# Optimization experiments

Measured on AMD Instinct MI355X. Metric: run time of the kernel, lower is better.

Reference implementation:

```python
import jax, jax.numpy as jnp
import numpy as np

ALPHABET = 26
VGENES = 60
JGENES = 20
E = 1024      # embedding_dim (= 2*VJ + LATENT)
H = 2048      # hidden_dim
LATENT = 768  # latent_space_dim
VJ = 128      # embedding_dim_VJ
L = 4096      # sequence length
X_IDX = 23    # all_letters.index('X')
B_IDX = 1     # all_letters.index('B')


def setup_inputs() -> dict:
    key = jax.random.key(0)
    ks = jax.random.split(key, 16)
    s = lambda fan_in: 1.0 / np.sqrt(fan_in)
    u = lambda k, shape, sc: jax.random.uniform(k, shape, jnp.float32, -sc, sc)
    return {
        "x": jax.random.randint(ks[0], (L,), 0, ALPHABET, dtype=jnp.int32),
        "Vg": jax.random.randint(ks[1], (1,), 0, VGENES, dtype=jnp.int32),
        "Jg": jax.random.randint(ks[2], (1,), 0, JGENES, dtype=jnp.int32),
        "tick": 0,
        "emb": jax.random.normal(ks[3], (ALPHABET, E), jnp.float32),
        "embV": jax.random.normal(ks[4], (VGENES, VJ), jnp.float32),
        "embJ": jax.random.normal(ks[5], (JGENES, VJ), jnp.float32),
        "W_ih_enc": u(ks[6], (4 * H, E), s(H)),
        "W_hh_enc": u(ks[7], (4 * H, H), s(H)),
        "b_ih_enc": u(ks[8], (4 * H,), s(H)),
        "b_hh_enc": u(ks[9], (4 * H,), s(H)),
        "W_ls": u(ks[10], (LATENT, H), s(H)),
        "b_ls": u(ks[11], (LATENT,), s(H)),
        "W_ih_dec": u(ks[12], (4 * E, E), s(E)),
        "W_hh_dec": u(ks[13], (4 * E, E), s(E)),
        "b_ih_dec": u(ks[14], (4 * E,), s(E)),
        "b_hh_dec": u(ks[15], (4 * E,), s(E)),
    }


def _lstm_cell(x_t, h, c, W_ih, W_hh, b):
    # torch gate order: i, f, g, o
    g = x_t @ W_ih.T + h @ W_hh.T + b
    i, f, gg, o = jnp.split(g, 4, axis=-1)
    c = jax.nn.sigmoid(f) * c + jax.nn.sigmoid(i) * jnp.tanh(gg)
    h = jax.nn.sigmoid(o) * jnp.tanh(c)
    return h, c


def reference(x, Vg, Jg, tick, emb, embV, embJ,
              W_ih_enc, W_hh_enc, b_ih_enc, b_hh_enc,
              W_ls, b_ls,
              W_ih_dec, W_hh_dec, b_ih_dec, b_hh_dec):
    # ---- encode ----
    embedded = emb[x]                       # [L, E]
    b_enc = b_ih_enc + b_hh_enc

    def enc_step(carry, x_t):
        h, c = carry
        h, c = _lstm_cell(x_t, h, c, W_ih_enc, W_hh_enc, b_enc)
        return (h, c), None

    h0 = jnp.zeros((H,), embedded.dtype)
    (h_n, _), _ = jax.lax.scan(enc_step, (h0, h0), embedded)
    latent = jnp.tanh(h_n @ W_ls.T + b_ls)  # [LATENT]

    # ---- concat latent with V/J gene embeddings -> [E] ----
    latent_cat = jnp.concatenate([embV[Vg[0]], latent, embJ[Jg[0]]])

    # ---- decode: feed own output back as next input ----
    b_dec = b_ih_dec + b_hh_dec
    prev0 = emb[X_IDX]                      # start letter embedding [E]

    def dec_step(carry, _):
        prev, h, c = carry
        h, c = _lstm_cell(prev, h, c, W_ih_dec, W_hh_dec, b_dec)
        return (h, h, c), h

    (_, _, _), outs = jax.lax.scan(dec_step, (prev0, latent_cat, latent_cat),
                                   None, length=L - 2)  # [L-2, E]

    seq = jnp.concatenate([prev0[None], outs, emb[B_IDX][None]], axis=0)  # [L, E]
    recon = seq[::-1][:, None, :]           # [L, 1, E] (original reverses the list)

    return latent_cat[None, None, :], recon, embedded
```

## Files before the change

### kernel.cpp

```cpp
#include <hip/hip_runtime.h>
#include <hip/hip_bf16.h>
#include <stdint.h>

#define NWG 256
typedef unsigned long long u64;

typedef __attribute__((ext_vector_type(8))) short bf16x8;
typedef __attribute__((ext_vector_type(4))) float f32x4;

__device__ __forceinline__ short f2bf(float f) {
    unsigned u = __float_as_uint(f);
    unsigned r = (u + 0x7fffu + ((u >> 16) & 1u)) >> 16;
    return (short)r;
}

__device__ __forceinline__ void gload16(const void* g, void* l) {
    __builtin_amdgcn_global_load_lds(
        (const __attribute__((address_space(1))) void*)g,
        (__attribute__((address_space(3))) void*)l, 16, 0, 0);
}

__device__ __forceinline__ u64 ald(const u64* p) {
    return __hip_atomic_load(p, __ATOMIC_RELAXED, __HIP_MEMORY_SCOPE_AGENT);
}
__device__ __forceinline__ void ast(u64* p, u64 v) {
    __hip_atomic_store(p, v, __ATOMIC_RELAXED, __HIP_MEMORY_SCOPE_AGENT);
}
__device__ __forceinline__ u64 pack(unsigned tag, float f) {
    return ((u64)tag << 32) | (u64)(unsigned)__float_as_uint(f);
}

__global__ void prep_all(const int* __restrict__ x, const int* __restrict__ Vg, const int* __restrict__ Jg,
                         const float* __restrict__ emb, const float* __restrict__ embV, const float* __restrict__ embJ,
                         const float* __restrict__ Wih_e,
                         const float* __restrict__ Wih_d, const float* __restrict__ Whh_d,
                         float* __restrict__ out,
                         short* __restrict__ Abf, short* __restrict__ Wbf,
                         float* __restrict__ wsum,
                         u64* __restrict__ bufE, u64* __restrict__ bufD)
{
    const size_t i0 = (size_t)blockIdx.x * blockDim.x + threadIdx.x;
    const size_t str = (size_t)gridDim.x * blockDim.x;
    for (size_t i = i0; i < (size_t)4096 * 1024; i += str) {
        int t = (int)(i >> 10), j = (int)(i & 1023);
        float v = emb[(size_t)x[t] * 1024 + j];
        out[4195328 + i] = v;
        Abf[i] = f2bf(v);
    }
    for (size_t i = i0; i < (size_t)8192 * 1024; i += str) Wbf[i] = f2bf(Wih_e[i]);
    for (size_t i = i0; i < (size_t)4096 * 1024; i += str) wsum[i] = Wih_d[i] + Whh_d[i];
    for (size_t i = i0; i < 1024; i += str) {
        out[1024 + i] = emb[1 * 1024 + i];
        out[1024 + (size_t)4095 * 1024 + i] = emb[23 * 1024 + i];
    }
    for (size_t i = i0; i < 6144; i += str) bufE[i] = 0ull;
    for (size_t i = i0; i < 3072; i += str) {
        u64 v = 0ull;
        if (i < 1024) {
            if (i < 128)      v = pack(0u, embV[(size_t)Vg[0] * 128 + i]);
            else if (i < 896) v = 0xFFFFFFFF00000000ull;
            else              v = pack(0u, embJ[(size_t)Jg[0] * 128 + (i - 896)]);
        }
        bufD[i] = v;
    }
    for (size_t i = i0; i < 128; i += str) {
        out[i]       = embV[(size_t)Vg[0] * 128 + i];
        out[896 + i] = embJ[(size_t)Jg[0] * 128 + i];
    }
}

__global__ void prep_pg(const float* __restrict__ Wih_d, const float* __restrict__ emb,
                        const float* __restrict__ bih_d, const float* __restrict__ bhh_d,
                        float* __restrict__ pg)
{
    const int lane = threadIdx.x & 63, wv = threadIdx.x >> 6;
    const float* prev0 = emb + 23 * 1024;
    for (int rr = 0; rr < 16; rr++) {
        int row = blockIdx.x * 64 + wv * 16 + rr;
        float s = 0.f;
        #pragma unroll
        for (int q = 0; q < 16; q++) {
            int k = lane + q * 64;
            s += Wih_d[(size_t)row * 1024 + k] * prev0[k];
        }
        for (int o = 32; o; o >>= 1) s += __shfl_xor(s, o, 64);
        if (lane == 0) pg[row] = s + bih_d[row] + bhh_d[row];
    }
}

__launch_bounds__(256, 2)
__global__ void gemm_xgates(const short* __restrict__ A,
                            const short* __restrict__ B,
                            const float* __restrict__ bih, const float* __restrict__ bhh,
                            float* __restrict__ C)
{
    __shared__ short lA[128 * 32];
    __shared__ short lB[128 * 32];
    const int bid = blockIdx.x;
    const int mb = bid >> 6;
    const int nb = bid & 63;
    const int tid = threadIdx.x, lane = tid & 63, wv = tid >> 6;
    const int wr = wv >> 1, wc = wv & 1;
    const int Mbase = mb * 128, Nbase = nb * 128;
    f32x4 acc[4][4] = {};

    for (int kt = 0; kt < 32; kt++) {
        __syncthreads();
        const int k0b = kt * 64;
        #pragma unroll
        for (int c = 0; c < 2; c++) {
            int f = tid * 16 + c * 4096;
            int row = f >> 6, kb = f & 63;
            const char* ga = (const char*)A + (size_t)(Mbase + row) * 2048 + k0b + kb;
            const char* gb = (const char*)B + (size_t)(Nbase + row) * 2048 + k0b + kb;
            gload16(ga, (char*)lA + wv * 1024 + c * 4096);
            gload16(gb, (char*)lB + wv * 1024 + c * 4096);
        }
        asm volatile("s_waitcnt vmcnt(0)" ::: "memory");
        __syncthreads();
        bf16x8 af[4], bf[4];
        #pragma unroll
        for (int i = 0; i < 4; i++) {
            af[i] = *(const bf16x8*)&lA[(wr * 64 + i * 16 + (lane & 15)) * 32 + (lane >> 4) * 8];
            bf[i] = *(const bf16x8*)&lB[(wc * 64 + i * 16 + (lane & 15)) * 32 + (lane >> 4) * 8];
        }
        #pragma unroll
        for (int i = 0; i < 4; i++)
            #pragma unroll
            for (int j = 0; j < 4; j++)
                acc[i][j] = __builtin_amdgcn_mfma_f32_16x16x32_bf16(af[i], bf[j], acc[i][j], 0, 0, 0);
    }
    #pragma unroll
    for (int i = 0; i < 4; i++) {
        #pragma unroll
        for (int j = 0; j < 4; j++) {
            int col = Nbase + wc * 64 + j * 16 + (lane & 15);
            float bv = bih[col] + bhh[col];
            #pragma unroll
            for (int r = 0; r < 4; r++) {
                int row = Mbase + wr * 64 + i * 16 + (lane >> 4) * 4 + r;
                C[(size_t)row * 8192 + col] = acc[i][j][r] + bv;
            }
        }
    }
}

__launch_bounds__(1024, 4)
__global__ void rnn_seq(const float* __restrict__ Whh_e,
                        const float* __restrict__ Wls,
                        const float* __restrict__ bls,
                        const float* __restrict__ Whh_d,
                        const float* __restrict__ Gx,
                        const float* __restrict__ wsum,
                        const float* __restrict__ bih_d, const float* __restrict__ bhh_d,
                        const float* __restrict__ pg,
                        u64* __restrict__ bufE,
                        u64* __restrict__ bufD,
                        float* __restrict__ out)
{
    const int w = blockIdx.x;
    const int tid = threadIdx.x;
    const int lane = tid & 63, wv = tid >> 6;
    __shared__ float hl[2][2048];
    __shared__ float red[2][32];
    __shared__ float cst[8];

    float we[64];
    #pragma unroll
    for (int rr = 0; rr < 2; rr++) {
        int r = wv * 2 + rr;
        const float* src = Whh_e + (size_t)((r >> 3) * 2048 + 8 * w + (r & 7)) * 2048 + lane;
        #pragma unroll
        for (int j = 0; j < 32; j++) we[rr * 32 + j] = src[64 * j];
    }
    if (tid < 8) cst[tid] = 0.f;
    const int grow = (tid >> 3) * 2048 + 8 * w + (tid & 7);
    float gx = 0.f;
    if (tid < 32) gx = Gx[grow];
    __syncthreads();

    #pragma unroll 1
    for (int t = 0; t < 4096; t++) {
        const unsigned tg = (unsigned)t;
        const u64* p = bufE + (size_t)(t % 3) * 2048 + wv * 128 + 2 * lane;
        u64 a0 = ald(p), a1 = ald(p + 1);
        for (;;) {
            bool ok = ((unsigned)(a0 >> 32) == tg) & ((unsigned)(a1 >> 32) == tg);
            if (__builtin_expect(__all(ok), 1)) break;
            a0 = ald(p); a1 = ald(p + 1);
        }
        float2 hv = { __uint_as_float((unsigned)a0), __uint_as_float((unsigned)a1) };
        *(float2*)&hl[t & 1][wv * 128 + 2 * lane] = hv;
        __syncthreads();

        float gx_next = 0.f;
        if (tid < 32 && t < 4095) gx_next = Gx[(size_t)(t + 1) * 8192 + grow];

        float s0 = 0.f, s1 = 0.f;
        const float* hp = hl[t & 1];
        #pragma unroll
        for (int j = 0; j < 32; j++) {
            float h = hp[lane + 64 * j];
            s0 += we[j] * h;
            s1 += we[32 + j] * h;
        }
        #pragma unroll
        for (int o = 32; o; o >>= 1) {
            s0 += __shfl_xor(s0, o, 64);
            s1 += __shfl_xor(s1, o, 64);
        }
        if (lane == 0) { red[t & 1][wv * 2] = s0; red[t & 1][wv * 2 + 1] = s1; }
        __syncthreads();

        if (tid < 32) {
            float g = red[t & 1][tid] + gx;
            float gi = __shfl(g, (tid & 7), 64);
            float gf = __shfl(g, (tid & 7) + 8, 64);
            float gg = __shfl(g, (tid & 7) + 16, 64);
            float go = __shfl(g, (tid & 7) + 24, 64);
            if (tid < 8) {
                float c  = cst[tid];
                float ig = 1.f / (1.f + expf(-gi));
                float fg = 1.f / (1.f + expf(-gf));
                float og = 1.f / (1.f + expf(-go));
                float cn = fg * c + ig * tanhf(gg);
                float hn = og * tanhf(cn);
                cst[tid] = cn;
                ast(&bufE[(size_t)((t + 1) % 3) * 2048 + 8 * w + tid], pack(tg + 1, hn));
            }
        }
        gx = gx_next;
    }

    {
        const unsigned tg = 4096u;
        const u64* p = bufE + (size_t)2048 + wv * 128 + 2 * lane;
        u64 a0 = ald(p), a1 = ald(p + 1);
        for (;;) {
            bool ok = ((unsigned)(a0 >> 32) == tg) & ((unsigned)(a1 >> 32) == tg);
            if (__builtin_expect(__all(ok), 1)) break;
            a0 = ald(p); a1 = ald(p + 1);
        }
        float2 hv = { __uint_as_float((unsigned)a0), __uint_as_float((unsigned)a1) };
        *(float2*)&hl[0][wv * 128 + 2 * lane] = hv;
        __syncthreads();

        if (wv < 3) {
            int row = 3 * w + wv;
            const float* wr = Wls + (size_t)row * 2048;
            float s = 0.f;
            #pragma unroll
            for (int q = 0; q < 32; q++) s += wr[lane + 64 * q] * hl[0][lane + 64 * q];
            for (int o = 32; o; o >>= 1) s += __shfl_xor(s, o, 64);
            if (lane == 0) {
                float lv = tanhf(s + bls[row]);
                out[128 + row] = lv;
                ast(&bufD[128 + row], pack(0u, lv));
            }
        }
        __syncthreads();
    }

    const int Rd = (wv >> 2) * 1024 + 4 * w + (wv & 3);
    float wd[16];
    {
        const float* src = wsum + (size_t)Rd * 1024 + lane;
        #pragma unroll
        for (int j = 0; j < 16; j++) wd[j] = src[64 * j];
    }
    float bdv = 0.f, pgv = 0.f;
    if (tid < 16) {
        int R = (tid >> 2) * 1024 + 4 * w + (tid & 3);
        bdv = bih_d[R] + bhh_d[R];
        pgv = pg[R];
    }
    if (tid < 8) cst[tid] = 0.f;
    if (tid < 4) {
        const u64* pc = bufD + 4 * w + tid;
        u64 v;
        do { v = ald(pc); } while ((unsigned)(v >> 32) != 0u);
        cst[tid] = __uint_as_float((unsigned)v);
    }
    __syncthreads();

    #pragma unroll 1
    for (int s = 1; s <= 4094; s++) {
        const unsigned tg = (unsigned)(s - 1);
        const u64* p = bufD + (size_t)((s - 1) % 3) * 1024 + wv * 64 + lane;
        u64 a0 = ald(p);
        for (;;) {
            bool ok = ((unsigned)(a0 >> 32) == tg);
            if (__builtin_expect(__all(ok), 1)) break;
            a0 = ald(p);
        }
        hl[(s - 1) & 1][wv * 64 + lane] = __uint_as_float((unsigned)a0);
        __syncthreads();

        float s0 = 0.f;
        const float* hp = hl[(s - 1) & 1];
        if (s == 1) {
            const float* srcw = Whh_d + (size_t)Rd * 1024 + lane;
            #pragma unroll
            for (int j = 0; j < 16; j++) s0 += srcw[64 * j] * hp[lane + 64 * j];
        } else {
            #pragma unroll
            for (int j = 0; j < 16; j++) s0 += wd[j] * hp[lane + 64 * j];
        }
        #pragma unroll
        for (int o = 32; o; o >>= 1) s0 += __shfl_xor(s0, o, 64);
        if (lane == 0) red[(s - 1) & 1][wv] = s0;
        __syncthreads();

        if (tid < 16) {
            float g = red[(s - 1) & 1][tid] + ((s == 1) ? pgv : bdv);
            float gi = __shfl(g, (tid & 3), 64);
            float gf = __shfl(g, (tid & 3) + 4, 64);
            float gg = __shfl(g, (tid & 3) + 8, 64);
            float go = __shfl(g, (tid & 3) + 12, 64);
            if (tid < 4) {
                float c  = cst[tid];
                float ig = 1.f / (1.f + expf(-gi));
                float fg = 1.f / (1.f + expf(-gf));
                float og = 1.f / (1.f + expf(-go));
                float cn = fg * c + ig * tanhf(gg);
                float hn = og * tanhf(cn);
                cst[tid] = cn;
                out[1024 + (size_t)(4095 - s) * 1024 + 4 * w + tid] = hn;
                ast(&bufD[(size_t)(s % 3) * 1024 + 4 * w + tid], pack((unsigned)s, hn));
            }
        }
    }
}

extern "C" void kernel_launch(void* const* d_in, const int* in_sizes, int n_in,
                              void* d_out, int out_size, void* d_ws, size_t ws_size,
                              hipStream_t stream)
{
    const int* x      = (const int*)d_in[0];
    const int* Vg     = (const int*)d_in[1];
    const int* Jg     = (const int*)d_in[2];
    const float* emb   = (const float*)d_in[4];
    const float* embV  = (const float*)d_in[5];
    const float* embJ  = (const float*)d_in[6];
    const float* Wih_e = (const float*)d_in[7];
    const float* Whh_e = (const float*)d_in[8];
    const float* bih_e = (const float*)d_in[9];
    const float* bhh_e = (const float*)d_in[10];
    const float* Wls   = (const float*)d_in[11];
    const float* bls   = (const float*)d_in[12];
    const float* Wih_d = (const float*)d_in[13];
    const float* Whh_d = (const float*)d_in[14];
    const float* bih_d = (const float*)d_in[15];
    const float* bhh_d = (const float*)d_in[16];
    float* out = (float*)d_out;

    char* ws = (char*)d_ws;
    u64*   bufE = (u64*)ws;
    u64*   bufD = (u64*)(ws + 49152);
    float* pg   = (float*)(ws + 73728);
    short* Abf  = (short*)(ws + 90368);
    short* Wbf  = (short*)(ws + 8478976);
    float* wsum = (float*)(ws + 25256192);
    float* Gx   = (float*)(ws + 42033408);

    prep_all<<<1024, 256, 0, stream>>>(x, Vg, Jg, emb, embV, embJ,
                                       Wih_e, Wih_d, Whh_d,
                                       out, Abf, Wbf, wsum, bufE, bufD);
    prep_pg<<<64, 256, 0, stream>>>(Wih_d, emb, bih_d, bhh_d, pg);
    gemm_xgates<<<2048, 256, 0, stream>>>(Abf, Wbf, bih_e, bhh_e, Gx);

    void* args[] = { (void*)&Whh_e, (void*)&Wls, (void*)&bls, (void*)&Whh_d,
                     (void*)&Gx, (void*)&wsum, (void*)&bih_d, (void*)&bhh_d, (void*)&pg,
                     (void*)&bufE, (void*)&bufD, (void*)&out };
    hipLaunchCooperativeKernel((const void*)rnn_seq, dim3(NWG), dim3(1024), args, 0, stream);
}
```

Baseline: 24.93 ms.

## Pack hidden-state exchange into 32-bit bf16+tag words, halve threads, batch Gx prefetch

The hidden state exchanged between workgroups each step is now packed as a 16-bit tag plus a bf16 value in a 32-bit word instead of a 64-bit tag+fp32. This halves the bytes each block polls from global memory per timestep. The block size drops from 1024 to 512 threads, so each wave holds twice as many weight rows in registers and the block-level syncs and reductions get cheaper. Input-gate precomputes are prefetched 64 timesteps at a time into LDS with async global-to-LDS loads. The bf16 hidden state loses precision in the recurrence, and the 16-bit tag only just covers the 4096 steps.

```diff
diff --git a/kernel.cpp b/kernel.cpp
--- a/kernel.cpp
+++ b/kernel.cpp
@@ -8,11 +8,11 @@
 typedef __attribute__((ext_vector_type(8))) short bf16x8;
 typedef __attribute__((ext_vector_type(4))) float f32x4;
 
-__device__ __forceinline__ short f2bf(float f) {
+__device__ __forceinline__ unsigned f2bfu(float f) {
     unsigned u = __float_as_uint(f);
-    unsigned r = (u + 0x7fffu + ((u >> 16) & 1u)) >> 16;
-    return (short)r;
-}
+    return (u + 0x7fffu + ((u >> 16) & 1u)) >> 16;
+}
+__device__ __forceinline__ short f2bf(float f) { return (short)f2bfu(f); }
 
 __device__ __forceinline__ void gload16(const void* g, void* l) {
     __builtin_amdgcn_global_load_lds(
@@ -20,14 +20,17 @@
         (__attribute__((address_space(3))) void*)l, 16, 0, 0);
 }
 
-__device__ __forceinline__ u64 ald(const u64* p) {
+__device__ __forceinline__ unsigned aldu(const unsigned* p) {
     return __hip_atomic_load(p, __ATOMIC_RELAXED, __HIP_MEMORY_SCOPE_AGENT);
 }
-__device__ __forceinline__ void ast(u64* p, u64 v) {
+__device__ __forceinline__ void astu(unsigned* p, unsigned v) {
     __hip_atomic_store(p, v, __ATOMIC_RELAXED, __HIP_MEMORY_SCOPE_AGENT);
 }
-__device__ __forceinline__ u64 pack(unsigned tag, float f) {
-    return ((u64)tag << 32) | (u64)(unsigned)__float_as_uint(f);
+__device__ __forceinline__ unsigned packh(unsigned tag, float f) {
+    return (tag << 16) | f2bfu(f);
+}
+__device__ __forceinline__ float unpackh(unsigned v) {
+    return __uint_as_float(v << 16);
 }
 
 __global__ void prep_all(const int* __restrict__ x, const int* __restrict__ Vg, const int* __restrict__ Jg,
@@ -37,7 +40,7 @@
                          float* __restrict__ out,
                          short* __restrict__ Abf, short* __restrict__ Wbf,
                          float* __restrict__ wsum,
-                         u64* __restrict__ bufE, u64* __restrict__ bufD)
+                         unsigned* __restrict__ bufE, unsigned* __restrict__ bufD)
 {
     const size_t i0 = (size_t)blockIdx.x * blockDim.x + threadIdx.x;
     const size_t str = (size_t)gridDim.x * blockDim.x;
@@ -53,13 +56,13 @@
         out[1024 + i] = emb[1 * 1024 + i];
         out[1024 + (size_t)4095 * 1024 + i] = emb[23 * 1024 + i];
     }
-    for (size_t i = i0; i < 6144; i += str) bufE[i] = 0ull;
+    for (size_t i = i0; i < 6144; i += str) bufE[i] = 0u;
     for (size_t i = i0; i < 3072; i += str) {
-        u64 v = 0ull;
+        unsigned v = 0u;
         if (i < 1024) {
-            if (i < 128)      v = pack(0u, embV[(size_t)Vg[0] * 128 + i]);
-            else if (i < 896) v = 0xFFFFFFFF00000000ull;
-            else              v = pack(0u, embJ[(size_t)Jg[0] * 128 + (i - 896)]);
+            if (i < 128)      v = packh(0u, embV[(size_t)Vg[0] * 128 + i]);
+            else if (i < 896) v = 0xFFFF0000u;
+            else              v = packh(0u, embJ[(size_t)Jg[0] * 128 + (i - 896)]);
         }
         bufD[i] = v;
     }
@@ -145,7 +148,7 @@
     }
 }
 
-__launch_bounds__(1024, 4)
+__launch_bounds__(512, 2)
 __global__ void rnn_seq(const float* __restrict__ Whh_e,
                         const float* __restrict__ Wls,
                         const float* __restrict__ bls,
@@ -154,66 +157,75 @@
                         const float* __restrict__ wsum,
                         const float* __restrict__ bih_d, const float* __restrict__ bhh_d,
                         const float* __restrict__ pg,
-                        u64* __restrict__ bufE,
-                        u64* __restrict__ bufD,
+                        unsigned* __restrict__ bufE,
+                        unsigned* __restrict__ bufD,
                         float* __restrict__ out)
 {
     const int w = blockIdx.x;
     const int tid = threadIdx.x;
     const int lane = tid & 63, wv = tid >> 6;
     __shared__ float hl[2][2048];
+    __shared__ float hlG[2][2048];
     __shared__ float red[2][32];
     __shared__ float cst[8];
 
-    float we[64];
+    float we[128];
     #pragma unroll
-    for (int rr = 0; rr < 2; rr++) {
-        int r = wv * 2 + rr;
+    for (int rr = 0; rr < 4; rr++) {
+        int r = wv * 4 + rr;
         const float* src = Whh_e + (size_t)((r >> 3) * 2048 + 8 * w + (r & 7)) * 2048 + lane;
         #pragma unroll
         for (int j = 0; j < 32; j++) we[rr * 32 + j] = src[64 * j];
     }
     if (tid < 8) cst[tid] = 0.f;
-    const int grow = (tid >> 3) * 2048 + 8 * w + (tid & 7);
-    float gx = 0.f;
-    if (tid < 32) gx = Gx[grow];
     __syncthreads();
+
+    const size_t gxsrc_off = ((size_t)((tid & 7) >> 1)) * 2048 + 8 * w + (tid & 1) * 4;
 
     #pragma unroll 1
     for (int t = 0; t < 4096; t++) {
+        if ((t & 63) == 0) {
+            int buf = (t >> 6) & 1;
+            const float* src = Gx + (size_t)(t + (tid >> 3)) * 8192 + gxsrc_off;
+            gload16(src, (char*)hlG + buf * 8192 + wv * 1024);
+        }
+
         const unsigned tg = (unsigned)t;
-        const u64* p = bufE + (size_t)(t % 3) * 2048 + wv * 128 + 2 * lane;
-        u64 a0 = ald(p), a1 = ald(p + 1);
+        const unsigned* p = bufE + (size_t)(t % 3) * 2048 + wv * 256 + 4 * lane;
+        unsigned a0 = aldu(p), a1 = aldu(p + 1), a2 = aldu(p + 2), a3 = aldu(p + 3);
         for (;;) {
-            bool ok = ((unsigned)(a0 >> 32) == tg) & ((unsigned)(a1 >> 32) == tg);
+            bool ok = ((a0 >> 16) == tg) & ((a1 >> 16) == tg)
+                    & ((a2 >> 16) == tg) & ((a3 >> 16) == tg);
             if (__builtin_expect(__all(ok), 1)) break;
-            a0 = ald(p); a1 = ald(p + 1);
-        }
-        float2 hv = { __uint_as_float((unsigned)a0), __uint_as_float((unsigned)a1) };
-        *(float2*)&hl[t & 1][wv * 128 + 2 * lane] = hv;
-        __syncthreads();
-
-        float gx_next = 0.f;
-        if (tid < 32 && t < 4095) gx_next = Gx[(size_t)(t + 1) * 8192 + grow];
-
-        float s0 = 0.f, s1 = 0.f;
+            a0 = aldu(p); a1 = aldu(p + 1); a2 = aldu(p + 2); a3 = aldu(p + 3);
+        }
+        float4 hv = { unpackh(a0), unpackh(a1), unpackh(a2), unpackh(a3) };
+        *(float4*)&hl[t & 1][wv * 256 + 4 * lane] = hv;
+        __syncthreads();
+
+        float s0 = 0.f, s1 = 0.f, s2 = 0.f, s3 = 0.f;
         const float* hp = hl[t & 1];
         #pragma unroll
         for (int j = 0; j < 32; j++) {
             float h = hp[lane + 64 * j];
             s0 += we[j] * h;
             s1 += we[32 + j] * h;
+            s2 += we[64 + j] * h;
+            s3 += we[96 + j] * h;
         }
         #pragma unroll
         for (int o = 32; o; o >>= 1) {
-            s0 += __shfl_xor(s0, o, 64);
-            s1 += __shfl_xor(s1, o, 64);
-        }
-        if (lane == 0) { red[t & 1][wv * 2] = s0; red[t & 1][wv * 2 + 1] = s1; }
+            s0 += __shfl_xor(s0, o, 64); s1 += __shfl_xor(s1, o, 64);
+            s2 += __shfl_xor(s2, o, 64); s3 += __shfl_xor(s3, o, 64);
+        }
+        if (lane == 0) {
+            red[t & 1][wv * 4]     = s0; red[t & 1][wv * 4 + 1] = s1;
+            red[t & 1][wv * 4 + 2] = s2; red[t & 1][wv * 4 + 3] = s3;
+        }
         __syncthreads();
 
         if (tid < 32) {
-            float g = red[t & 1][tid] + gx;
+            float g = red[t & 1][tid] + hlG[(t >> 6) & 1][(t & 63) * 32 + tid];
             float gi = __shfl(g, (tid & 7), 64);
             float gf = __shfl(g, (tid & 7) + 8, 64);
             float gg = __shfl(g, (tid & 7) + 16, 64);
@@ -226,23 +238,23 @@
                 float cn = fg * c + ig * tanhf(gg);
                 float hn = og * tanhf(cn);
                 cst[tid] = cn;
-                ast(&bufE[(size_t)((t + 1) % 3) * 2048 + 8 * w + tid], pack(tg + 1, hn));
-            }
-        }
-        gx = gx_next;
+                astu(&bufE[(size_t)((t + 1) % 3) * 2048 + 8 * w + tid], packh(tg + 1, hn));
+            }
+        }
     }
 
     {
         const unsigned tg = 4096u;
-        const u64* p = bufE + (size_t)2048 + wv * 128 + 2 * lane;
-        u64 a0 = ald(p), a1 = ald(p + 1);
+        const unsigned* p = bufE + (size_t)2048 + wv * 256 + 4 * lane;
+        unsigned a0 = aldu(p), a1 = aldu(p + 1), a2 = aldu(p + 2), a3 = aldu(p + 3);
         for (;;) {
-            bool ok = ((unsigned)(a0 >> 32) == tg) & ((unsigned)(a1 >> 32) == tg);
+            bool ok = ((a0 >> 16) == tg) & ((a1 >> 16) == tg)
+                    & ((a2 >> 16) == tg) & ((a3 >> 16) == tg);
             if (__builtin_expect(__all(ok), 1)) break;
-            a0 = ald(p); a1 = ald(p + 1);
-        }
-        float2 hv = { __uint_as_float((unsigned)a0), __uint_as_float((unsigned)a1) };
-        *(float2*)&hl[0][wv * 128 + 2 * lane] = hv;
+            a0 = aldu(p); a1 = aldu(p + 1); a2 = aldu(p + 2); a3 = aldu(p + 3);
+        }
+        float4 hv = { unpackh(a0), unpackh(a1), unpackh(a2), unpackh(a3) };
+        *(float4*)&hl[0][wv * 256 + 4 * lane] = hv;
         __syncthreads();
 
         if (wv < 3) {
@@ -255,18 +267,19 @@
             if (lane == 0) {
                 float lv = tanhf(s + bls[row]);
                 out[128 + row] = lv;
-                ast(&bufD[128 + row], pack(0u, lv));
-            }
-        }
-        __syncthreads();
-    }
-
-    const int Rd = (wv >> 2) * 1024 + 4 * w + (wv & 3);
-    float wd[16];
-    {
-        const float* src = wsum + (size_t)Rd * 1024 + lane;
-        #pragma unroll
-        for (int j = 0; j < 16; j++) wd[j] = src[64 * j];
+                astu(&bufD[128 + row], packh(0u, lv));
+            }
+        }
+        __syncthreads();
+    }
+
+    float wd[32];
+    #pragma unroll
+    for (int rr = 0; rr < 2; rr++) {
+        int r = wv * 2 + rr;
+        const float* src = wsum + (size_t)((r >> 2) * 1024 + 4 * w + (r & 3)) * 1024 + lane;
+        #pragma unroll
+        for (int j = 0; j < 16; j++) wd[rr * 16 + j] = src[64 * j];
     }
     float bdv = 0.f, pgv = 0.f;
     if (tid < 16) {
@@ -276,39 +289,53 @@
     }
     if (tid < 8) cst[tid] = 0.f;
     if (tid < 4) {
-        const u64* pc = bufD + 4 * w + tid;
-        u64 v;
-        do { v = ald(pc); } while ((unsigned)(v >> 32) != 0u);
-        cst[tid] = __uint_as_float((unsigned)v);
+        const unsigned* pc = bufD + 4 * w + tid;
+        unsigned v;
+        do { v = aldu(pc); } while ((v >> 16) != 0u);
+        cst[tid] = unpackh(v);
     }
     __syncthreads();
 
     #pragma unroll 1
     for (int s = 1; s <= 4094; s++) {
         const unsigned tg = (unsigned)(s - 1);
-        const u64* p = bufD + (size_t)((s - 1) % 3) * 1024 + wv * 64 + lane;
-        u64 a0 = ald(p);
+        const unsigned* p = bufD + (size_t)((s - 1) % 3) * 1024 + wv * 128 + 2 * lane;
+        unsigned a0 = aldu(p), a1 = aldu(p + 1);
         for (;;) {
-            bool ok = ((unsigned)(a0 >> 32) == tg);
+            bool ok = ((a0 >> 16) == tg) & ((a1 >> 16) == tg);
             if (__builtin_expect(__all(ok), 1)) break;
-            a0 = ald(p);
-        }
-        hl[(s - 1) & 1][wv * 64 + lane] = __uint_as_float((unsigned)a0);
-        __syncthreads();
-
-        float s0 = 0.f;
+            a0 = aldu(p); a1 = aldu(p + 1);
+        }
+        float2 hv = { unpackh(a0), unpackh(a1) };
+        *(float2*)&hl[(s - 1) & 1][wv * 128 + 2 * lane] = hv;
+        __syncthreads();
+
+        float s0 = 0.f, s1 = 0.f;
         const float* hp = hl[(s - 1) & 1];
         if (s == 1) {
-            const float* srcw = Whh_d + (size_t)Rd * 1024 + lane;
             #pragma unroll
-            for (int j = 0; j < 16; j++) s0 += srcw[64 * j] * hp[lane + 64 * j];
+            for (int rr = 0; rr < 2; rr++) {
+                int r = wv * 2 + rr;
+                const float* srcw = Whh_d + (size_t)((r >> 2) * 1024 + 4 * w + (r & 3)) * 1024 + lane;
+                float a = 0.f;
+                #pragma unroll
+                for (int j = 0; j < 16; j++) a += srcw[64 * j] * hp[lane + 64 * j];
+                if (rr) s1 = a; else s0 = a;
+            }
         } else {
             #pragma unroll
-            for (int j = 0; j < 16; j++) s0 += wd[j] * hp[lane + 64 * j];
-        }
-        #pragma unroll
-        for (int o = 32; o; o >>= 1) s0 += __shfl_xor(s0, o, 64);
-        if (lane == 0) red[(s - 1) & 1][wv] = s0;
+            for (int j = 0; j < 16; j++) {
+                float h = hp[lane + 64 * j];
+                s0 += wd[j] * h;
+                s1 += wd[16 + j] * h;
+            }
+        }
+        #pragma unroll
+        for (int o = 32; o; o >>= 1) {
+            s0 += __shfl_xor(s0, o, 64);
+            s1 += __shfl_xor(s1, o, 64);
+        }
+        if (lane == 0) { red[(s - 1) & 1][wv * 2] = s0; red[(s - 1) & 1][wv * 2 + 1] = s1; }
         __syncthreads();
 
         if (tid < 16) {
@@ -326,7 +353,7 @@
                 float hn = og * tanhf(cn);
                 cst[tid] = cn;
                 out[1024 + (size_t)(4095 - s) * 1024 + 4 * w + tid] = hn;
-                ast(&bufD[(size_t)(s % 3) * 1024 + 4 * w + tid], pack((unsigned)s, hn));
+                astu(&bufD[(size_t)(s % 3) * 1024 + 4 * w + tid], packh((unsigned)s, hn));
             }
         }
     }
@@ -355,9 +382,9 @@
     float* out = (float*)d_out;
 
     char* ws = (char*)d_ws;
-    u64*   bufE = (u64*)ws;
-    u64*   bufD = (u64*)(ws + 49152);
-    float* pg   = (float*)(ws + 73728);
+    unsigned* bufE = (unsigned*)ws;
+    unsigned* bufD = (unsigned*)(ws + 24576);
+    float* pg   = (float*)(ws + 36864);
     short* Abf  = (short*)(ws + 90368);
     short* Wbf  = (short*)(ws + 8478976);
     float* wsum = (float*)(ws + 25256192);
@@ -372,5 +399,5 @@
     void* args[] = { (void*)&Whh_e, (void*)&Wls, (void*)&bls, (void*)&Whh_d,
                      (void*)&Gx, (void*)&wsum, (void*)&bih_d, (void*)&bhh_d, (void*)&pg,
                      (void*)&bufE, (void*)&bufD, (void*)&out };
-    hipLaunchCooperativeKernel((const void*)rnn_seq, dim3(NWG), dim3(1024), args, 0, stream);
-}
+    hipLaunchCooperativeKernel((const void*)rnn_seq, dim3(NWG), dim3(512), args, 0, stream);
+}
```

Measured after the change: 28.72 ms. 15.2% more time.
